# Kernel optimization log

Measured on AMD Instinct MI355X. Metric: run time of the kernel, lower is better.

The kernel has to match this reference:

```python
import jax, jax.numpy as jnp
import numpy as np

PATCH_SIZE = 2  # init arg patch_size


def setup_inputs() -> dict:
    key = jax.random.key(0)
    k1, k2, k3, k4, k5 = jax.random.split(key, 5)
    b, H, W, d = 8, 32, 32, 256
    n_obj = 15
    patches = jax.random.normal(k1, (b, H, W, d), jnp.float32)
    embs = jax.random.normal(k2, (b, n_obj, 256), jnp.float32)
    locations = jax.random.randint(k3, (b, n_obj, 4), 0, 32, jnp.int32)
    Wp = jax.random.normal(k4, (256, 256), jnp.float32) * 0.05
    We = jax.random.normal(k5, (256, 256), jnp.float32) * 0.05
    return {"patches": patches, "embs": embs, "locations": locations, "Wp": Wp, "We": We}


def _build_masks(locations, b, H, W):
    # patching(): floor starts / ceil ends to multiples of PATCH_SIZE
    starts = locations[..., :2] - locations[..., :2] % PATCH_SIZE
    ends = locations[..., 2:] + (PATCH_SIZE - locations[..., 2:] % PATCH_SIZE)
    locs = jnp.concatenate([starts, ends], axis=-1)          # [b, n_obj, 4]
    img = jnp.broadcast_to(jnp.array([0, 0, H, W], locs.dtype), (b, 1, 4))
    locs = jnp.concatenate([locs, img], axis=1)              # [b, n, 4]
    rows = jnp.arange(H)[:, None]                             # [H,1]
    cols = jnp.arange(W)[None, :]                             # [1,W]
    y0 = locs[..., 0, None, None]; x0 = locs[..., 1, None, None]
    y1 = locs[..., 2, None, None]; x1 = locs[..., 3, None, None]
    # vectorized box rasterization (replaces torch slice-assign scatter loops)
    m = (rows >= y0) & (rows < y1) & (cols >= x0) & (cols < x1)  # [b,n,H,W]
    return m.reshape(b, locs.shape[1], H * W)                 # [b,n,HW]


def reference(patches, embs, locations, Wp, We):
    b, H, W, d = patches.shape
    # append mean embedding (torch: cat([embs, embs.mean(dim=1, keepdim=True)]))
    embs = jnp.concatenate([embs, embs.mean(axis=1, keepdims=True)], axis=1)  # [b,n,e]
    masks = _build_masks(locations, b, H, W)                  # [b,n,HW] bool
    mf = masks.astype(patches.dtype)
    # InjectionBlock (assumed minimal): project patches, inject masked emb
    proj = jnp.einsum('bpd,do->bpo', patches.reshape(b, H * W, d), Wp)  # [b,HW,o]
    inj = jnp.einsum('bne,eo->bno', embs, We)                 # [b,n,o]
    p = proj[:, None] + mf[..., None] * inj[:, :, None, :]    # [b,n,HW,o]
    # masked mean pooling over the n mask channels
    out = (p * mf[..., None]).sum(axis=1) / mf.sum(axis=1)[..., None]  # [b,HW,o]
    return out
```

## Files before the change

kernel.cpp:

```cpp
#include <hip/hip_runtime.h>
#include <hip/hip_bf16.h>

typedef short short8 __attribute__((ext_vector_type(8)));
typedef float f32x4 __attribute__((ext_vector_type(4)));

static __device__ __forceinline__ ushort2 pk2(float a, float b) {
    __hip_bfloat162 h = __float22bfloat162_rn(make_float2(a, b));
    ushort2 r;
    __builtin_memcpy(&r, &h, 4);
    return r;
}
static __device__ __forceinline__ unsigned short bf1(float a) {
    __hip_bfloat16 h = __float2bfloat16(a);
    unsigned short r;
    __builtin_memcpy(&r, &h, 2);
    return r;
}

__global__ __launch_bounds__(256)
void fused_all(const float* __restrict__ patches,
               const float* __restrict__ embs,
               const int* __restrict__ locations,
               const float* __restrict__ Wp,
               const float* __restrict__ We,
               float* __restrict__ out) {
    __shared__ __align__(16) unsigned short Ash[64 * 256];
    __shared__ __align__(16) unsigned short Ebf[16 * 256];
    __shared__ unsigned maskL[64];
    __shared__ float rcL[64];

    const int bid = blockIdx.x, t = threadIdx.x;
    const int b = bid >> 6, pt = (bid >> 2) & 15, ct = bid & 3;
    const int p0 = pt * 64, c0 = ct * 64;
    const int wv = t >> 6, lane = t & 63, lhi = lane >> 4, llo = lane & 15;
    const int oc = c0 + wv * 16 + llo;

    const float* pbase = patches + (size_t)(b * 1024 + p0) * 256;
    #pragma unroll
    for (int it = 0; it < 16; ++it) {
        int u = t + it * 256;
        int row = u >> 6, c4 = u & 63;
        float4 f = *reinterpret_cast<const float4*>(pbase + row * 256 + c4 * 4);
        ushort2 lo = pk2(f.x, f.y), hi = pk2(f.z, f.w);
        ushort4 o = {lo.x, lo.y, hi.x, hi.y};
        int byte = row * 512 + ((c4 * 8) ^ ((row & 7) << 4));
        *reinterpret_cast<ushort4*>(reinterpret_cast<char*>(Ash) + byte) = o;
    }

    if (t < 128) {
        const int c0e = t * 2;
        float s0 = 0.f, s1 = 0.f;
        #pragma unroll
        for (int r = 0; r < 15; ++r) {
            float2 v = *reinterpret_cast<const float2*>(embs + (size_t)(b * 15 + r) * 256 + c0e);
            s0 += v.x; s1 += v.y;
            ushort2 p2 = pk2(v.x, v.y);
            unsigned pk = (unsigned)p2.x | ((unsigned)p2.y << 16);
            *reinterpret_cast<unsigned*>(reinterpret_cast<char*>(Ebf)
                + r * 512 + ((c0e * 2) ^ ((r & 7) << 4))) = pk;
        }
        ushort2 p2 = pk2(s0 * (1.0f / 15.0f), s1 * (1.0f / 15.0f));
        unsigned pk = (unsigned)p2.x | ((unsigned)p2.y << 16);
        *reinterpret_cast<unsigned*>(reinterpret_cast<char*>(Ebf)
            + 15 * 512 + ((c0e * 2) ^ (7 << 4))) = pk;
    }

    if (t < 64) {
        int p = p0 + t;
        int h = p >> 5, w = p & 31;
        const int* loc = locations + b * 60;
        unsigned m = 1u << 15;
        #pragma unroll
        for (int nb = 0; nb < 15; ++nb) {
            int y0 = loc[nb * 4 + 0] & ~1;
            int x0 = loc[nb * 4 + 1] & ~1;
            int y1 = (loc[nb * 4 + 2] & ~1) + 2;
            int x1 = (loc[nb * 4 + 3] & ~1) + 2;
            if (h >= y0 && h < y1 && w >= x0 && w < x1) m |= 1u << nb;
        }
        maskL[t] = m;
        rcL[t] = 1.0f / (float)__popc(m);
    }
    __syncthreads();

    f32x4 accI = (f32x4){0.f, 0.f, 0.f, 0.f};
    #pragma unroll
    for (int ks = 0; ks < 8; ++ks) {
        const short8 afr = *reinterpret_cast<const short8*>(
            reinterpret_cast<const char*>(Ebf)
            + llo * 512 + ((ks * 64 + lhi * 16) ^ ((llo & 7) << 4)));
        short8 bfr;
        #pragma unroll
        for (int rr = 0; rr < 4; ++rr) {
            float w0 = We[(size_t)(ks * 32 + lhi * 8 + 2 * rr + 0) * 256 + oc];
            float w1 = We[(size_t)(ks * 32 + lhi * 8 + 2 * rr + 1) * 256 + oc];
            ushort2 p2 = pk2(w0, w1);
            bfr[2 * rr + 0] = (short)p2.x;
            bfr[2 * rr + 1] = (short)p2.y;
        }
        accI = __builtin_amdgcn_mfma_f32_16x16x32_bf16(afr, bfr, accI, 0, 0, 0);
    }
    short8 jf;
    {
        ushort2 plo = pk2(accI[0], accI[1]);
        ushort2 phi = pk2(accI[2], accI[3]);
        int q0 = (int)((unsigned)plo.x | ((unsigned)plo.y << 16));
        int q1 = (int)((unsigned)phi.x | ((unsigned)phi.y << 16));
        int a0 = (llo + 32 * lhi) << 2;
        union { short8 s; int i[4]; } J;
        J.i[0] = __builtin_amdgcn_ds_bpermute(a0, q0);
        J.i[1] = __builtin_amdgcn_ds_bpermute(a0, q1);
        J.i[2] = __builtin_amdgcn_ds_bpermute(a0 + 64, q0);
        J.i[3] = __builtin_amdgcn_ds_bpermute(a0 + 64, q1);
        jf = J.s;
    }

    f32x4 acc[4];
    #pragma unroll
    for (int mt = 0; mt < 4; ++mt) acc[mt] = (f32x4){0.f, 0.f, 0.f, 0.f};
    #pragma unroll
    for (int ks = 0; ks < 8; ++ks) {
        short8 bfr;
        #pragma unroll
        for (int rr = 0; rr < 4; ++rr) {
            float w0 = Wp[(size_t)(ks * 32 + lhi * 8 + 2 * rr + 0) * 256 + oc];
            float w1 = Wp[(size_t)(ks * 32 + lhi * 8 + 2 * rr + 1) * 256 + oc];
            ushort2 p2 = pk2(w0, w1);
            bfr[2 * rr + 0] = (short)p2.x;
            bfr[2 * rr + 1] = (short)p2.y;
        }
        #pragma unroll
        for (int mt = 0; mt < 4; ++mt) {
            int row = mt * 16 + llo;
            const short8 af = *reinterpret_cast<const short8*>(
                reinterpret_cast<const char*>(Ash)
                + row * 512 + (((ks * 32 + lhi * 8) * 2) ^ ((row & 7) << 4)));
            acc[mt] = __builtin_amdgcn_mfma_f32_16x16x32_bf16(af, bfr, acc[mt], 0, 0, 0);
        }
    }

    #pragma unroll
    for (int mt = 0; mt < 4; ++mt) {
        unsigned m = maskL[mt * 16 + llo];
        unsigned short rcb = bf1(rcL[mt * 16 + llo]);
        short8 mfrag;
        #pragma unroll
        for (int r = 0; r < 8; ++r) {
            int k = lhi * 8 + r;
            mfrag[r] = (k < 16 && ((m >> k) & 1u)) ? (short)rcb : (short)0;
        }
        f32x4 accE = __builtin_amdgcn_mfma_f32_16x16x32_bf16(
            mfrag, jf, (f32x4){0.f, 0.f, 0.f, 0.f}, 0, 0, 0);
        float* ob = out + (size_t)(b * 1024 + p0 + mt * 16) * 256;
        #pragma unroll
        for (int j = 0; j < 4; ++j)
            ob[(lhi * 4 + j) * 256 + oc] = acc[mt][j] + accE[j];
    }
}

extern "C" void kernel_launch(void* const* d_in, const int* in_sizes, int n_in,
                              void* d_out, int out_size, void* d_ws, size_t ws_size,
                              hipStream_t stream) {
    const float* patches = (const float*)d_in[0];
    const float* embs    = (const float*)d_in[1];
    const int*   locs    = (const int*)d_in[2];
    const float* Wp      = (const float*)d_in[3];
    const float* We      = (const float*)d_in[4];
    float* out = (float*)d_out;

    fused_all<<<512, 256, 0, stream>>>(patches, embs, locs, Wp, We, out);
}
```

Before: 16.19 us.

## Load embeddings directly to registers and fold mean-row into mask coefficients

Patches are loaded into registers early, and their bf16 conversion and LDS store are deferred until after the injection MFMA, so global latency overlaps with the We GEMM. The embedding LDS staging buffer is dropped: each lane reads its embedding row straight from global memory, and the mean-embedding row is zeroed. Its contribution is folded algebraically into the mask coefficients (rc*16/15 for set bits, rc/15 otherwise). This removes one LDS round trip and a barrier, at the cost of higher register pressure (16 float4 per thread) and slightly different bf16 rounding.

```diff
diff --git a/kernel.cpp b/kernel.cpp
--- a/kernel.cpp
+++ b/kernel.cpp
@@ -25,7 +25,6 @@
                const float* __restrict__ We,
                float* __restrict__ out) {
     __shared__ __align__(16) unsigned short Ash[64 * 256];
-    __shared__ __align__(16) unsigned short Ebf[16 * 256];
     __shared__ unsigned maskL[64];
     __shared__ float rcL[64];
 
@@ -36,33 +35,12 @@
     const int oc = c0 + wv * 16 + llo;
 
     const float* pbase = patches + (size_t)(b * 1024 + p0) * 256;
+    float4 areg[16];
     #pragma unroll
     for (int it = 0; it < 16; ++it) {
         int u = t + it * 256;
         int row = u >> 6, c4 = u & 63;
-        float4 f = *reinterpret_cast<const float4*>(pbase + row * 256 + c4 * 4);
-        ushort2 lo = pk2(f.x, f.y), hi = pk2(f.z, f.w);
-        ushort4 o = {lo.x, lo.y, hi.x, hi.y};
-        int byte = row * 512 + ((c4 * 8) ^ ((row & 7) << 4));
-        *reinterpret_cast<ushort4*>(reinterpret_cast<char*>(Ash) + byte) = o;
-    }
-
-    if (t < 128) {
-        const int c0e = t * 2;
-        float s0 = 0.f, s1 = 0.f;
-        #pragma unroll
-        for (int r = 0; r < 15; ++r) {
-            float2 v = *reinterpret_cast<const float2*>(embs + (size_t)(b * 15 + r) * 256 + c0e);
-            s0 += v.x; s1 += v.y;
-            ushort2 p2 = pk2(v.x, v.y);
-            unsigned pk = (unsigned)p2.x | ((unsigned)p2.y << 16);
-            *reinterpret_cast<unsigned*>(reinterpret_cast<char*>(Ebf)
-                + r * 512 + ((c0e * 2) ^ ((r & 7) << 4))) = pk;
-        }
-        ushort2 p2 = pk2(s0 * (1.0f / 15.0f), s1 * (1.0f / 15.0f));
-        unsigned pk = (unsigned)p2.x | ((unsigned)p2.y << 16);
-        *reinterpret_cast<unsigned*>(reinterpret_cast<char*>(Ebf)
-            + 15 * 512 + ((c0e * 2) ^ (7 << 4))) = pk;
+        areg[it] = *reinterpret_cast<const float4*>(pbase + row * 256 + c4 * 4);
     }
 
     if (t < 64) {
@@ -81,14 +59,21 @@
         maskL[t] = m;
         rcL[t] = 1.0f / (float)__popc(m);
     }
-    __syncthreads();
 
+    const float* erow = embs + (size_t)(b * 15 + (llo < 15 ? llo : 0)) * 256;
+    const bool ez = (llo == 15);
     f32x4 accI = (f32x4){0.f, 0.f, 0.f, 0.f};
     #pragma unroll
     for (int ks = 0; ks < 8; ++ks) {
-        const short8 afr = *reinterpret_cast<const short8*>(
-            reinterpret_cast<const char*>(Ebf)
-            + llo * 512 + ((ks * 64 + lhi * 16) ^ ((llo & 7) << 4)));
+        float4 e0 = *reinterpret_cast<const float4*>(erow + ks * 32 + lhi * 8);
+        float4 e1 = *reinterpret_cast<const float4*>(erow + ks * 32 + lhi * 8 + 4);
+        ushort2 pa = pk2(e0.x, e0.y), pb = pk2(e0.z, e0.w);
+        ushort2 pc = pk2(e1.x, e1.y), pd = pk2(e1.z, e1.w);
+        short8 afr;
+        afr[0] = ez ? 0 : (short)pa.x; afr[1] = ez ? 0 : (short)pa.y;
+        afr[2] = ez ? 0 : (short)pb.x; afr[3] = ez ? 0 : (short)pb.y;
+        afr[4] = ez ? 0 : (short)pc.x; afr[5] = ez ? 0 : (short)pc.y;
+        afr[6] = ez ? 0 : (short)pd.x; afr[7] = ez ? 0 : (short)pd.y;
         short8 bfr;
         #pragma unroll
         for (int rr = 0; rr < 4; ++rr) {
@@ -114,6 +99,18 @@
         J.i[3] = __builtin_amdgcn_ds_bpermute(a0 + 64, q1);
         jf = J.s;
     }
+
+    #pragma unroll
+    for (int it = 0; it < 16; ++it) {
+        int u = t + it * 256;
+        int row = u >> 6, c4 = u & 63;
+        float4 f = areg[it];
+        ushort2 lo = pk2(f.x, f.y), hi = pk2(f.z, f.w);
+        ushort4 o = {lo.x, lo.y, hi.x, hi.y};
+        int byte = row * 512 + ((c4 * 8) ^ ((row & 7) << 4));
+        *reinterpret_cast<ushort4*>(reinterpret_cast<char*>(Ash) + byte) = o;
+    }
+    __syncthreads();
 
     f32x4 acc[4];
     #pragma unroll
@@ -142,12 +139,14 @@
     #pragma unroll
     for (int mt = 0; mt < 4; ++mt) {
         unsigned m = maskL[mt * 16 + llo];
-        unsigned short rcb = bf1(rcL[mt * 16 + llo]);
+        float rc = rcL[mt * 16 + llo];
+        unsigned short rcA = bf1(rc * (16.0f / 15.0f));
+        unsigned short rcB = bf1(rc * (1.0f / 15.0f));
         short8 mfrag;
         #pragma unroll
         for (int r = 0; r < 8; ++r) {
             int k = lhi * 8 + r;
-            mfrag[r] = (k < 16 && ((m >> k) & 1u)) ? (short)rcb : (short)0;
+            mfrag[r] = (k < 15) ? (short)(((m >> k) & 1u) ? rcA : rcB) : (short)0;
         }
         f32x4 accE = __builtin_amdgcn_mfma_f32_16x16x32_bf16(
             mfrag, jf, (f32x4){0.f, 0.f, 0.f, 0.f}, 0, 0, 0);
```

After: 17.39 us. 1.07x slower.
